# Performance work log

Hardware: AMD Instinct MI355X
Metric: run time of the kernel (lower is better)

The kernel has to match this reference:

```python
import jax, jax.numpy as jnp
import numpy as np

B, T, C = 2, 2048, 2048
H = 16
D = C // H  # head_dim = 128
ROPE_BASE = 10000.0


def rope_cos_sin(seq_len, dim, dtype):
    inv_freq = 1.0 / (ROPE_BASE ** (jnp.arange(0, dim, 2, dtype=jnp.float32) / dim))
    t = jnp.arange(seq_len, dtype=jnp.float32)
    freqs = jnp.outer(t, inv_freq)              # [T, D/2]
    emb = jnp.concatenate([freqs, freqs], -1)   # [T, D]
    return emb.astype(dtype), None  # placeholder replaced below


def rotate_half(x):
    x1, x2 = jnp.split(x, 2, axis=-1)
    return jnp.concatenate([-x2, x1], axis=-1)


def setup_inputs() -> dict:
    key = jax.random.key(0)
    k1, k2, k3 = jax.random.split(key, 3)
    sc = 1.0 / np.sqrt(C)
    x = jax.random.normal(k1, (B, T, C), dtype=jnp.float32)
    w_qkv = jax.random.normal(k2, (C, 3 * C), dtype=jnp.float32) * sc
    w_out = jax.random.normal(k3, (C, C), dtype=jnp.float32) * sc
    return {"x": x, "w_qkv": w_qkv, "w_out": w_out}


def reference(x, w_qkv, w_out):
    Bq, Tq, Cq = x.shape
    qkv = x @ w_qkv                                    # [B,T,3C]
    q, k, v = jnp.split(qkv, 3, axis=-1)
    # [B,T,C] -> [B,H,T,D]
    q = q.reshape(Bq, Tq, H, D).transpose(0, 2, 1, 3)
    k = k.reshape(Bq, Tq, H, D).transpose(0, 2, 1, 3)
    v = v.reshape(Bq, Tq, H, D).transpose(0, 2, 1, 3)
    # RoPE
    inv_freq = 1.0 / (ROPE_BASE ** (jnp.arange(0, D, 2, dtype=jnp.float32) / D))
    freqs = jnp.outer(jnp.arange(Tq, dtype=jnp.float32), inv_freq)  # [T, D/2]
    emb = jnp.concatenate([freqs, freqs], -1)                        # [T, D]
    cos = jnp.cos(emb).astype(x.dtype)[None, None]                   # [1,1,T,D]
    sin = jnp.sin(emb).astype(x.dtype)[None, None]
    q = q * cos + rotate_half(q) * sin
    k = k * cos + rotate_half(k) * sin
    # causal SDPA
    scale = 1.0 / np.sqrt(D)
    att = jnp.einsum("bhqd,bhkd->bhqk", q, k) * scale
    causal = jnp.tril(jnp.ones((Tq, Tq), dtype=bool))
    att = jnp.where(causal[None, None], att, -jnp.inf)
    att = jax.nn.softmax(att, axis=-1)
    y = jnp.einsum("bhqk,bhkd->bhqd", att, v)          # [B,H,T,D]
    y = y.transpose(0, 2, 1, 3).reshape(Bq, Tq, Cq)
    return y @ w_out
```

## Files before the change

### kernel.cpp

```cpp
#include <hip/hip_runtime.h>
#include <hip/hip_bf16.h>
#include <type_traits>
#include <utility>

typedef unsigned short u16;
typedef unsigned int u32;

#define B_ 2
#define T_ 2048
#define C_ 2048
#define H_ 16
#define D_ 128
#define LDQKV 6144

typedef float float4v __attribute__((ext_vector_type(4)));
typedef short short8 __attribute__((ext_vector_type(8)));

__device__ inline u16 f2bf(float f) {
  u32 u = __builtin_bit_cast(u32, f);
  u32 r = u + 0x7fffu + ((u >> 16) & 1u);
  return (u16)(r >> 16);
}
__device__ inline float bfbits2f(u16 b) {
  return __builtin_bit_cast(float, (u32)b << 16);
}
__device__ inline u32 pack2bf(float a, float b) {
  u32 ua = (__builtin_bit_cast(u32, a) + 0x8000u) >> 16;
  u32 ub = (__builtin_bit_cast(u32, b) + 0x8000u) & 0xffff0000u;
  return ua | ub;
}

#if defined(__HIP_DEVICE_COMPILE__)
typedef __bf16 bf16x8 __attribute__((ext_vector_type(8)));

template <typename V, typename = void>
struct mfma_takes_short : std::false_type {};
template <typename V>
struct mfma_takes_short<V, std::void_t<decltype(__builtin_amdgcn_mfma_f32_16x16x32_bf16(
    std::declval<V>(), std::declval<V>(), std::declval<float4v>(), 0, 0, 0))>>
    : std::true_type {};

template <typename SV>
__device__ inline float4v mfma_bf16(SV a, SV b, float4v c) {
  if constexpr (mfma_takes_short<SV>::value) {
    return __builtin_amdgcn_mfma_f32_16x16x32_bf16(a, b, c, 0, 0, 0);
  } else {
    return __builtin_amdgcn_mfma_f32_16x16x32_bf16(
        __builtin_bit_cast(bf16x8, a), __builtin_bit_cast(bf16x8, b), c, 0, 0, 0);
  }
}

__device__ inline void async16(u16* lds, const u16* g) {
  typedef __attribute__((address_space(3))) void lds_void;
  typedef __attribute__((address_space(1))) const void g_void;
  __builtin_amdgcn_global_load_lds((g_void*)g, (lds_void*)lds, 16, 0, 0);
}
#endif

__global__ __launch_bounds__(256) void cast_f32_bf16(const float* __restrict__ s,
                                                     u16* __restrict__ d) {
  int i = (blockIdx.x * 256 + threadIdx.x) * 4;
  float4 v = *(const float4*)(s + i);
  alignas(8) u16 o[4] = {f2bf(v.x), f2bf(v.y), f2bf(v.z), f2bf(v.w)};
  *(uint2*)(d + i) = *(const uint2*)o;
}

__global__ __launch_bounds__(256) void castT_f32_bf16(const float* __restrict__ src,
                                                      u16* __restrict__ dst,
                                                      int R, int Cc) {
  __shared__ float tile[32][33];
  const int t = threadIdx.x;
  const int r0 = blockIdx.y * 32, c0 = blockIdx.x * 32;
  const int lr = t >> 3, lc = (t & 7) * 4;
  float4 v = *(const float4*)(src + (size_t)(r0 + lr) * Cc + c0 + lc);
  tile[lr][lc + 0] = v.x;
  tile[lr][lc + 1] = v.y;
  tile[lr][lc + 2] = v.z;
  tile[lr][lc + 3] = v.w;
  __syncthreads();
  alignas(8) u16 o[4];
#pragma unroll
  for (int j = 0; j < 4; ++j) o[j] = f2bf(tile[lc + j][lr]);
  *(uint2*)(dst + (size_t)(c0 + lr) * R + r0 + lc) = *(const uint2*)o;
}

__global__ __launch_bounds__(256) void vT_build(const u16* __restrict__ qkv,
                                                u16* __restrict__ Vt) {
  __shared__ u16 lt[64][72];
  const int tid = threadIdx.x;
  const int bh = blockIdx.x;
  const int tt = blockIdx.y;
  const int dd = blockIdx.z;
  const int b = bh >> 4, h = bh & 15;
  const int r = tid >> 2;
  const int c4 = (tid & 3) * 16;
  const u16* src = qkv + ((size_t)(b * T_ + tt * 64 + r)) * LDQKV + 2 * C_ + h * 128 + dd * 64 + c4;
  *(uint4*)&lt[r][c4] = *(const uint4*)src;
  *(uint4*)&lt[r][c4 + 8] = *(const uint4*)(src + 8);
  __syncthreads();
  alignas(16) u16 o[16];
#pragma unroll
  for (int j = 0; j < 16; ++j) o[j] = lt[c4 + j][r];
  u16* dst = Vt + ((size_t)(bh * 128 + dd * 64 + r)) * 2048 + tt * 64 + c4;
  *(uint4*)dst = *(const uint4*)o;
  *(uint4*)(dst + 8) = *(const uint4*)(o + 8);
}

template <bool CF32>
__global__ __launch_bounds__(256) void gemm_bt(const u16* __restrict__ A,
                                               const u16* __restrict__ BT,
                                               void* __restrict__ Cp,
                                               int K, int lda, int ldbt, int ldc) {
#if defined(__HIP_DEVICE_COMPILE__)
  __shared__ u16 As[4096];
  __shared__ u16 Bs[4096];
  const int tid = threadIdx.x;
  const int lane = tid & 63;
  const int w = tid >> 6;
  const int wm = w & 1, wn = w >> 1;
  const int ml = lane & 15, qd = lane >> 4;
  const int m0 = blockIdx.y * 128, n0 = blockIdx.x * 128;
  const int sm = lane >> 2, sk = (lane & 3) * 8;
  const u16* gA[2];
  const u16* gB[2];
  u16 *lA[2], *lB[2];
#pragma unroll
  for (int r = 0; r < 2; ++r) {
    int seg = r * 4 + w;
    gA[r] = A + (size_t)(m0 + seg * 16 + sm) * lda + sk;
    gB[r] = BT + (size_t)(n0 + seg * 16 + sm) * ldbt + sk;
    lA[r] = As + seg * 512;
    lB[r] = Bs + seg * 512;
  }
  float4v acc[4][4] = {};
  for (int kk = 0; kk < K; kk += 32) {
    __syncthreads();
    async16(lA[0], gA[0] + kk);
    async16(lA[1], gA[1] + kk);
    async16(lB[0], gB[0] + kk);
    async16(lB[1], gB[1] + kk);
    __syncthreads();
    short8 a[4], b[4];
#pragma unroll
    for (int mt = 0; mt < 4; ++mt)
      a[mt] = *(const short8*)(As + (wm * 64 + mt * 16 + ml) * 32 + qd * 8);
#pragma unroll
    for (int nt = 0; nt < 4; ++nt)
      b[nt] = *(const short8*)(Bs + (wn * 64 + nt * 16 + ml) * 32 + qd * 8);
#pragma unroll
    for (int mt = 0; mt < 4; ++mt)
#pragma unroll
      for (int nt = 0; nt < 4; ++nt) acc[mt][nt] = mfma_bf16(a[mt], b[nt], acc[mt][nt]);
  }
#pragma unroll
  for (int mt = 0; mt < 4; ++mt) {
#pragma unroll
    for (int nt = 0; nt < 4; ++nt) {
#pragma unroll
      for (int r = 0; r < 4; ++r) {
        int row = m0 + wm * 64 + mt * 16 + qd * 4 + r;
        int col = n0 + wn * 64 + nt * 16 + ml;
        if constexpr (CF32) {
          ((float*)Cp)[(size_t)row * ldc + col] = acc[mt][nt][r];
        } else {
          ((u16*)Cp)[(size_t)row * ldc + col] = f2bf(acc[mt][nt][r]);
        }
      }
    }
  }
#endif
}

template <bool AF32, bool BF32, bool CF32>
__global__ __launch_bounds__(256) void gemm_mixed(const void* __restrict__ Ap,
                                                  const void* __restrict__ Bp,
                                                  void* __restrict__ Cp,
                                                  int M, int N, int K,
                                                  int lda, int ldb, int ldc) {
#if defined(__HIP_DEVICE_COMPILE__)
  __shared__ u16 As[64][40];
  __shared__ u16 Bs[64][40];
  const int tid = threadIdx.x;
  const int lane = tid & 63;
  const int w = tid >> 6;
  const int m0 = blockIdx.y * 64;
  const int n0 = blockIdx.x * 64;
  const int arow = tid >> 2, acol = (tid & 3) * 8;
  const int brow = tid >> 3, bcol = (tid & 7) * 8;
  const int ml = lane & 15, qd = lane >> 4;
  float4v acc[4] = {};
  for (int kk = 0; kk < K; kk += 32) {
    __syncthreads();
    if constexpr (AF32) {
      const float* A = (const float*)Ap;
      const float* src = A + (size_t)(m0 + arow) * lda + (kk + acol);
      float4 f0 = *(const float4*)src;
      float4 f1 = *(const float4*)(src + 4);
      alignas(16) u16 tmp[8] = {f2bf(f0.x), f2bf(f0.y), f2bf(f0.z), f2bf(f0.w),
                                f2bf(f1.x), f2bf(f1.y), f2bf(f1.z), f2bf(f1.w)};
      *(uint4*)(&As[arow][acol]) = *(const uint4*)tmp;
    } else {
      const u16* A = (const u16*)Ap;
      *(uint4*)(&As[arow][acol]) = *(const uint4*)(A + (size_t)(m0 + arow) * lda + (kk + acol));
    }
    if constexpr (BF32) {
      const float* Bm = (const float*)Bp;
      const float* src = Bm + (size_t)(kk + brow) * ldb + (n0 + bcol);
      float4 f0 = *(const float4*)src;
      float4 f1 = *(const float4*)(src + 4);
      float fv[8] = {f0.x, f0.y, f0.z, f0.w, f1.x, f1.y, f1.z, f1.w};
#pragma unroll
      for (int i = 0; i < 8; ++i) Bs[bcol + i][brow] = f2bf(fv[i]);
    } else {
      const u16* Bm = (const u16*)Bp;
      uint4 bv = *(const uint4*)(Bm + (size_t)(kk + brow) * ldb + (n0 + bcol));
      const u16* bsp = (const u16*)&bv;
#pragma unroll
      for (int i = 0; i < 8; ++i) Bs[bcol + i][brow] = bsp[i];
    }
    __syncthreads();
    short8 af = *(const short8*)(&As[w * 16 + ml][qd * 8]);
#pragma unroll
    for (int nt = 0; nt < 4; ++nt) {
      short8 bf = *(const short8*)(&Bs[nt * 16 + ml][qd * 8]);
      acc[nt] = mfma_bf16(af, bf, acc[nt]);
    }
  }
#pragma unroll
  for (int nt = 0; nt < 4; ++nt) {
#pragma unroll
    for (int r = 0; r < 4; ++r) {
      int row = m0 + w * 16 + qd * 4 + r;
      int col = n0 + nt * 16 + ml;
      if constexpr (CF32) {
        ((float*)Cp)[(size_t)row * ldc + col] = acc[nt][r];
      } else {
        ((u16*)Cp)[(size_t)row * ldc + col] = f2bf(acc[nt][r]);
      }
    }
  }
#endif
}

__global__ __launch_bounds__(256) void rope_inplace(u16* __restrict__ qkv, float qscale) {
  int idx = blockIdx.x * 256 + threadIdx.x;
  int d = idx & 63;
  int h = (idx >> 6) & 15;
  int t = (idx >> 10) & 2047;
  int b = idx >> 21;
  size_t row = (size_t)(b * T_ + t) * LDQKV;
  u16* qp = qkv + row + h * 128;
  u16* kp = qkv + row + C_ + h * 128;
  float q1 = bfbits2f(qp[d]);
  float q2 = bfbits2f(qp[d + 64]);
  float k1 = bfbits2f(kp[d]);
  float k2 = bfbits2f(kp[d + 64]);
  float invf = exp2f((float)d * -0.20762050593046012f);
  float fr = (float)t * invf;
  float sn, cs;
  sincosf(fr, &sn, &cs);
  qp[d] = f2bf((q1 * cs - q2 * sn) * qscale);
  qp[d + 64] = f2bf((q2 * cs + q1 * sn) * qscale);
  kp[d] = f2bf(k1 * cs - k2 * sn);
  kp[d + 64] = f2bf(k2 * cs + k1 * sn);
}

__global__ __launch_bounds__(256, 2) void attn_fwd2(u16* __restrict__ qkv,
                                                    const u16* __restrict__ Vt) {
#if defined(__HIP_DEVICE_COMPILE__)
  __shared__ alignas(16) u16 kS[64 * 128];
  __shared__ alignas(16) u16 vS[128 * 64];
  __shared__ alignas(16) u16 pS[4][32][72];
  const int tid = threadIdx.x;
  const int lane = tid & 63;
  const int w = tid >> 6;
  const int ml = lane & 15, qd = lane >> 4;
  const int gx = blockIdx.x;
  const int half = gx >> 8, rem = gx & 255;
  const int bh = rem >> 3, q3 = rem & 7;
  const int qt = half ? q3 : (15 - q3);
  const int b = bh >> 4, h = bh & 15;
  const int hc = h * 128;
  const int m0 = qt * 128;
  const size_t rb = (size_t)(b * T_);
  short8 qf[2][4];
#pragma unroll
  for (int m = 0; m < 2; ++m) {
    const u16* qp = qkv + (rb + m0 + w * 32 + m * 16 + ml) * LDQKV + hc;
#pragma unroll
    for (int k4 = 0; k4 < 4; ++k4) qf[m][k4] = *(const short8*)(qp + k4 * 32 + qd * 8);
  }
  float4v acc[2][8] = {};
  float mi[2] = {-1.0e30f, -1.0e30f}, li[2] = {0.f, 0.f};
  const int nchunk = 2 * qt + 2;
  const int krow0 = w * 16 + qd;
  const int vd0 = w * 32 + (lane >> 3);
  const int vsegoff = ((lane & 7) ^ (lane >> 3)) * 8;
  const size_t vtbase = ((size_t)bh * 128) * 2048;

  for (int c = 0; c < nchunk; ++c) {
    __syncthreads();
#pragma unroll
    for (int i = 0; i < 4; ++i) {
      int key = krow0 + i * 4;
      int seg = (ml ^ (i * 4 + qd)) * 8;
      async16(kS + (w * 4 + i) * 512,
              qkv + (rb + c * 64 + key) * LDQKV + C_ + hc + seg);
    }
#pragma unroll
    for (int i = 0; i < 4; ++i) {
      int d = vd0 + i * 8;
      async16(vS + (w * 4 + i) * 512,
              Vt + vtbase + (size_t)d * 2048 + c * 64 + vsegoff);
    }
    __syncthreads();
    if (c * 64 > m0 + w * 32 + 31) continue;
    float4v s[4][2] = {};
#pragma unroll
    for (int kt = 0; kt < 4; ++kt) {
#pragma unroll
      for (int k4 = 0; k4 < 4; ++k4) {
        int key = kt * 16 + ml;
        int slot = key * 16 + ((k4 * 4 + qd) ^ key);
        short8 kf = *(const short8*)(kS + ((kt * 16 + ml) * 16 + ((k4 * 4 + qd) ^ ml)) * 8);
        (void)key; (void)slot;
        s[kt][0] = mfma_bf16(kf, qf[0][k4], s[kt][0]);
        s[kt][1] = mfma_bf16(kf, qf[1][k4], s[kt][1]);
      }
    }
    const bool domask = (c * 64 + 63) > (m0 + w * 32);
    float alpha[2];
#pragma unroll
    for (int m = 0; m < 2; ++m) {
      int qrow = m0 + w * 32 + m * 16 + ml;
      if (domask) {
#pragma unroll
        for (int kt = 0; kt < 4; ++kt)
#pragma unroll
          for (int r = 0; r < 4; ++r) {
            int key = c * 64 + kt * 16 + qd * 4 + r;
            if (key > qrow) s[kt][m][r] = -1.0e30f;
          }
      }
      float mx = -1.0e30f;
#pragma unroll
      for (int kt = 0; kt < 4; ++kt)
#pragma unroll
        for (int r = 0; r < 4; ++r) mx = fmaxf(mx, s[kt][m][r]);
      mx = fmaxf(mx, __shfl_xor(mx, 16, 64));
      mx = fmaxf(mx, __shfl_xor(mx, 32, 64));
      float mnew = fmaxf(mi[m], mx);
      float a = __expf(mi[m] - mnew);
      float sm = 0.f;
#pragma unroll
      for (int kt = 0; kt < 4; ++kt)
#pragma unroll
        for (int r = 0; r < 4; ++r) {
          float p = __expf(s[kt][m][r] - mnew);
          s[kt][m][r] = p;
          sm += p;
        }
      sm += __shfl_xor(sm, 16, 64);
      sm += __shfl_xor(sm, 32, 64);
      li[m] = li[m] * a + sm;
      mi[m] = mnew;
      alpha[m] = a;
#pragma unroll
      for (int kt = 0; kt < 4; ++kt) {
        uint2 pk;
        pk.x = pack2bf(s[kt][m][0], s[kt][m][1]);
        pk.y = pack2bf(s[kt][m][2], s[kt][m][3]);
        *(uint2*)&pS[w][m * 16 + ml][kt * 16 + qd * 4] = pk;
      }
    }
#pragma unroll
    for (int m = 0; m < 2; ++m) {
#pragma unroll
      for (int r = 0; r < 4; ++r) {
        float aq = __shfl(alpha[m], qd * 4 + r, 64);
#pragma unroll
        for (int dt = 0; dt < 8; ++dt) acc[m][dt][r] *= aq;
      }
    }
#pragma unroll
    for (int k2 = 0; k2 < 2; ++k2) {
      short8 pa0 = *(const short8*)&pS[w][ml][k2 * 32 + qd * 8];
      short8 pa1 = *(const short8*)&pS[w][16 + ml][k2 * 32 + qd * 8];
#pragma unroll
      for (int dt = 0; dt < 8; ++dt) {
        int d = dt * 16 + ml;
        short8 vf = *(const short8*)(vS + (d * 8 + ((k2 * 4 + qd) ^ (ml & 7))) * 8);
        acc[0][dt] = mfma_bf16(pa0, vf, acc[0][dt]);
        acc[1][dt] = mfma_bf16(pa1, vf, acc[1][dt]);
      }
    }
  }
#pragma unroll
  for (int m = 0; m < 2; ++m) {
#pragma unroll
    for (int r = 0; r < 4; ++r) {
      float inv = 1.0f / __shfl(li[m], qd * 4 + r, 64);
      size_t row = rb + m0 + w * 32 + m * 16 + qd * 4 + r;
#pragma unroll
      for (int dt = 0; dt < 8; ++dt)
        qkv[row * LDQKV + hc + dt * 16 + ml] = f2bf(acc[m][dt][r] * inv);
    }
  }
#endif
}

__global__ __launch_bounds__(256, 2) void attn_fwd(u16* __restrict__ qkv) {
#if defined(__HIP_DEVICE_COMPILE__)
  __shared__ alignas(16) u16 ks[64][136];
  __shared__ alignas(16) u16 vt[128][72];
  __shared__ alignas(16) u16 pb[4][32][72];
  const int tid = threadIdx.x;
  const int lane = tid & 63;
  const int w = tid >> 6;
  const int ml = lane & 15, qd = lane >> 4;
  const int gx = blockIdx.x;
  const int half = gx >> 8;
  const int rem = gx & 255;
  const int bh = rem >> 3;
  const int q3 = rem & 7;
  const int qt = half ? q3 : (15 - q3);
  const int b = bh >> 4, h = bh & 15;
  const int hc = h * 128;
  const int m0 = qt * 128;
  const size_t rb = (size_t)(b * T_);
  short8 qf[2][4];
#pragma unroll
  for (int m = 0; m < 2; ++m) {
    const u16* qp = qkv + (rb + m0 + w * 32 + m * 16 + ml) * LDQKV + hc;
#pragma unroll
    for (int k4 = 0; k4 < 4; ++k4) qf[m][k4] = *(const short8*)(qp + k4 * 32 + qd * 8);
  }
  float4v acc[2][8] = {};
  float mi[2][4], li[2][4];
#pragma unroll
  for (int m = 0; m < 2; ++m)
#pragma unroll
    for (int r = 0; r < 4; ++r) { mi[m][r] = -1.0e30f; li[m][r] = 0.f; }
  const float scale = 0.08838834764831845f;
  const int srow = tid >> 2;
  const int scol = (tid & 3) * 32;
  const int nchunk = 2 * qt + 2;
  for (int c = 0; c < nchunk; ++c) {
    __syncthreads();
    {
      const u16* kp = qkv + (rb + c * 64 + srow) * LDQKV + C_ + hc + scol;
      const u16* vp = qkv + (rb + c * 64 + srow) * LDQKV + 2 * C_ + hc + scol;
#pragma unroll
      for (int i = 0; i < 4; ++i)
        *(uint4*)&ks[srow][scol + i * 8] = *(const uint4*)(kp + i * 8);
#pragma unroll
      for (int i = 0; i < 4; ++i) {
        uint4 vv = *(const uint4*)(vp + i * 8);
        const u16* e = (const u16*)&vv;
#pragma unroll
        for (int t = 0; t < 8; ++t) vt[scol + i * 8 + t][srow] = e[t];
      }
    }
    __syncthreads();
    if (c * 64 > m0 + w * 32 + 31) continue;
    float4v s[2][4] = {};
#pragma unroll
    for (int t = 0; t < 4; ++t) {
#pragma unroll
      for (int k4 = 0; k4 < 4; ++k4) {
        short8 bf = *(const short8*)(&ks[t * 16 + ml][k4 * 32 + qd * 8]);
        s[0][t] = mfma_bf16(qf[0][k4], bf, s[0][t]);
        s[1][t] = mfma_bf16(qf[1][k4], bf, s[1][t]);
      }
    }
    const bool domask = (c * 64 + 63) > (m0 + w * 32);
#pragma unroll
    for (int m = 0; m < 2; ++m) {
      float al[4];
#pragma unroll
      for (int r = 0; r < 4; ++r) {
        float x0 = s[m][0][r] * scale;
        float x1 = s[m][1][r] * scale;
        float x2 = s[m][2][r] * scale;
        float x3 = s[m][3][r] * scale;
        if (domask) {
          int row = m0 + w * 32 + m * 16 + qd * 4 + r;
          int j0 = c * 64 + ml;
          if (j0 > row) x0 = -1.0e30f;
          if (j0 + 16 > row) x1 = -1.0e30f;
          if (j0 + 32 > row) x2 = -1.0e30f;
          if (j0 + 48 > row) x3 = -1.0e30f;
        }
        float mx = fmaxf(fmaxf(x0, x1), fmaxf(x2, x3));
        mx = fmaxf(mx, __shfl_xor(mx, 1));
        mx = fmaxf(mx, __shfl_xor(mx, 2));
        mx = fmaxf(mx, __shfl_xor(mx, 4));
        mx = fmaxf(mx, __shfl_xor(mx, 8));
        float mnew = fmaxf(mi[m][r], mx);
        float a = __expf(mi[m][r] - mnew);
        float p0 = __expf(x0 - mnew);
        float p1 = __expf(x1 - mnew);
        float p2 = __expf(x2 - mnew);
        float p3 = __expf(x3 - mnew);
        float sm = p0 + p1 + p2 + p3;
        sm += __shfl_xor(sm, 1);
        sm += __shfl_xor(sm, 2);
        sm += __shfl_xor(sm, 4);
        sm += __shfl_xor(sm, 8);
        li[m][r] = li[m][r] * a + sm;
        mi[m][r] = mnew;
        al[r] = a;
        int prow = m * 16 + qd * 4 + r;
        pb[w][prow][ml] = f2bf(p0);
        pb[w][prow][16 + ml] = f2bf(p1);
        pb[w][prow][32 + ml] = f2bf(p2);
        pb[w][prow][48 + ml] = f2bf(p3);
      }
#pragma unroll
      for (int d = 0; d < 8; ++d) {
        acc[m][d][0] *= al[0];
        acc[m][d][1] *= al[1];
        acc[m][d][2] *= al[2];
        acc[m][d][3] *= al[3];
      }
    }
#pragma unroll
    for (int k2 = 0; k2 < 2; ++k2) {
      short8 pa0 = *(const short8*)(&pb[w][ml][k2 * 32 + qd * 8]);
      short8 pa1 = *(const short8*)(&pb[w][16 + ml][k2 * 32 + qd * 8]);
#pragma unroll
      for (int d = 0; d < 8; ++d) {
        short8 vf = *(const short8*)(&vt[d * 16 + ml][k2 * 32 + qd * 8]);
        acc[0][d] = mfma_bf16(pa0, vf, acc[0][d]);
        acc[1][d] = mfma_bf16(pa1, vf, acc[1][d]);
      }
    }
  }
#pragma unroll
  for (int m = 0; m < 2; ++m) {
#pragma unroll
    for (int r = 0; r < 4; ++r) {
      float inv = 1.0f / li[m][r];
      size_t row = rb + m0 + w * 32 + m * 16 + qd * 4 + r;
#pragma unroll
      for (int d = 0; d < 8; ++d)
        qkv[row * LDQKV + hc + d * 16 + ml] = f2bf(acc[m][d][r] * inv);
    }
  }
#endif
}

extern "C" void kernel_launch(void* const* d_in, const int* in_sizes, int n_in,
                              void* d_out, int out_size, void* d_ws, size_t ws_size,
                              hipStream_t stream) {
  const float* x = (const float*)d_in[0];
  const float* wqkv = (const float*)d_in[1];
  const float* wout = (const float*)d_in[2];
  float* out = (float*)d_out;
  char* ws = (char*)d_ws;
  u16* qkv = (u16*)ws;

  const size_t MB = 1024 * 1024;
  if (ws_size >= 96 * MB) {
    u16* xb = (u16*)(ws + 48 * MB);
    u16* wqkvT = (u16*)(ws + 64 * MB);
    u16* Vt = (u16*)(ws + 64 * MB);
    u16* woutT = (u16*)(ws + 88 * MB);
    cast_f32_bf16<<<dim3(8192), dim3(256), 0, stream>>>(x, xb);
    castT_f32_bf16<<<dim3(192, 64), dim3(256), 0, stream>>>(wqkv, wqkvT, 2048, 6144);
    castT_f32_bf16<<<dim3(64, 64), dim3(256), 0, stream>>>(wout, woutT, 2048, 2048);
    gemm_bt<false><<<dim3(48, 32), dim3(256), 0, stream>>>(
        xb, wqkvT, qkv, 2048, 2048, 2048, 6144);
    rope_inplace<<<dim3(16384), dim3(256), 0, stream>>>(qkv, 0.08838834764831845f);
    vT_build<<<dim3(32, 32, 2), dim3(256), 0, stream>>>(qkv, Vt);
    attn_fwd2<<<dim3(512), dim3(256), 0, stream>>>(qkv, Vt);
    gemm_bt<true><<<dim3(16, 32), dim3(256), 0, stream>>>(
        qkv, woutT, out, 2048, 6144, 2048, 2048);
  } else {
    gemm_mixed<true, true, false><<<dim3(96, 64), dim3(256), 0, stream>>>(
        x, wqkv, qkv, 4096, 6144, 2048, 2048, 6144, 6144);
    rope_inplace<<<dim3(16384), dim3(256), 0, stream>>>(qkv, 1.0f);
    attn_fwd<<<dim3(512), dim3(256), 0, stream>>>(qkv);
    gemm_mixed<false, true, true><<<dim3(32, 64), dim3(256), 0, stream>>>(
        qkv, wout, out, 4096, 2048, 2048, 6144, 2048, 2048);
  }
}
```

Before: 429.3 us.

## Add 256x256 ping-pong async-LDS GEMM for QKV projection

Replaces the 128x128-tile QKV projection GEMM with a new 256x256-tile kernel using 512 threads. It stages tiles through double-buffered shared memory via async global-to-LDS copies with XOR swizzling, and interleaves staging with MFMA under barriers and s_setprio. It also remaps workgroups with an XCD-aware swizzle. The aim is more data reuse per tile, with global-load latency hidden behind compute. The costs are 128 KB of LDS per block, which limits occupancy, and a grid of only 384 workgroups.

```diff
diff --git a/kernel.cpp b/kernel.cpp
--- a/kernel.cpp
+++ b/kernel.cpp
@@ -104,6 +104,164 @@
   u16* dst = Vt + ((size_t)(bh * 128 + dd * 64 + r)) * 2048 + tt * 64 + c4;
   *(uint4*)dst = *(const uint4*)o;
   *(uint4*)(dst + 8) = *(const uint4*)(o + 8);
+}
+
+template <bool CF32>
+__global__ __launch_bounds__(512, 2) void gemm256_bt(const u16* __restrict__ A,
+                                                     const u16* __restrict__ BT,
+                                                     void* __restrict__ Cp,
+                                                     int K, int lda, int ldbt, int ldc,
+                                                     int nbx) {
+#if defined(__HIP_DEVICE_COMPILE__)
+  __shared__ alignas(16) u16 As[2][256 * 64];
+  __shared__ alignas(16) u16 Bs[2][256 * 64];
+  const int tid = threadIdx.x;
+  const int lane = tid & 63;
+  const int w = tid >> 6;
+  const int wm = w >> 2, wn = w & 3;
+  const int ml = lane & 15, qd = lane >> 4;
+  const int nwg = gridDim.x;
+  const int cpx = nwg >> 3;
+  const int swz = (blockIdx.x & 7) * cpx + (blockIdx.x >> 3);
+  const int by = swz / nbx, bx = swz - by * nbx;
+  const int m0 = by * 256, n0 = bx * 256;
+  const int rowoff = lane >> 3;
+  const int chunk = ((lane & 7) ^ rowoff) * 8;
+  int rA0[2], rA1[2], rB0[2], rB1[2];
+#pragma unroll
+  for (int j = 0; j < 2; ++j) {
+    int g = w * 2 + j;
+    rA0[j] = (g >> 3) * 128 + (g & 7) * 8;
+    rA1[j] = (g >> 3) * 128 + 64 + (g & 7) * 8;
+    rB0[j] = (g >> 2) * 64 + (g & 3) * 8;
+    rB1[j] = (g >> 2) * 64 + 32 + (g & 3) * 8;
+  }
+  const int ntiles = K >> 6;
+  const int niter = ntiles >> 1;
+
+#define STG_A(bufi, h, kt)                                                       \
+  do {                                                                           \
+    async16(&As[bufi][rA##h[0] * 64],                                            \
+            A + (size_t)(m0 + rA##h[0] + rowoff) * lda + (kt) * 64 + chunk);     \
+    async16(&As[bufi][rA##h[1] * 64],                                            \
+            A + (size_t)(m0 + rA##h[1] + rowoff) * lda + (kt) * 64 + chunk);     \
+  } while (0)
+#define STG_B(bufi, h, kt)                                                       \
+  do {                                                                           \
+    async16(&Bs[bufi][rB##h[0] * 64],                                            \
+            BT + (size_t)(n0 + rB##h[0] + rowoff) * ldbt + (kt) * 64 + chunk);   \
+    async16(&Bs[bufi][rB##h[1] * 64],                                            \
+            BT + (size_t)(n0 + rB##h[1] + rowoff) * ldbt + (kt) * 64 + chunk);   \
+  } while (0)
+#define LDA8(bufi, mh)                                                           \
+  do {                                                                           \
+    _Pragma("unroll") for (int mt_ = 0; mt_ < 4; ++mt_)                          \
+    _Pragma("unroll") for (int ks_ = 0; ks_ < 2; ++ks_)                          \
+      a[mt_][ks_] = *(const short8*)&As[bufi][                                   \
+          (wm * 128 + (mh) * 64 + mt_ * 16 + ml) * 64 +                          \
+          (((qd + ks_ * 4) ^ (ml & 7)) * 8)];                                    \
+  } while (0)
+#define LDB4(bufi, nh)                                                           \
+  do {                                                                           \
+    _Pragma("unroll") for (int nt_ = 0; nt_ < 2; ++nt_)                          \
+    _Pragma("unroll") for (int ks_ = 0; ks_ < 2; ++ks_)                          \
+      b[nt_][ks_] = *(const short8*)&Bs[bufi][                                   \
+          (wn * 64 + (nh) * 32 + nt_ * 16 + ml) * 64 +                           \
+          (((qd + ks_ * 4) ^ (ml & 7)) * 8)];                                    \
+  } while (0)
+#define MMA16(mh, nh)                                                            \
+  do {                                                                           \
+    __builtin_amdgcn_s_setprio(1);                                               \
+    _Pragma("unroll") for (int ks_ = 0; ks_ < 2; ++ks_)                          \
+    _Pragma("unroll") for (int mt_ = 0; mt_ < 4; ++mt_)                          \
+    _Pragma("unroll") for (int nt_ = 0; nt_ < 2; ++nt_)                          \
+      acc[(mh) * 4 + mt_][(nh) * 2 + nt_] = mfma_bf16(                           \
+          a[mt_][ks_], b[nt_][ks_], acc[(mh) * 4 + mt_][(nh) * 2 + nt_]);        \
+    __builtin_amdgcn_s_setprio(0);                                               \
+  } while (0)
+#define BAR __builtin_amdgcn_s_barrier()
+#define LGKM0 asm volatile("s_waitcnt lgkmcnt(0)" ::: "memory")
+#define LGKM8 asm volatile("s_waitcnt lgkmcnt(8)" ::: "memory")
+#define VM4 asm volatile("s_waitcnt vmcnt(4)" ::: "memory")
+
+  float4v acc[8][4] = {};
+  short8 a[4][2], b[2][2];
+
+  STG_A(0, 0, 0);
+  STG_B(0, 0, 0);
+  STG_A(0, 1, 0);
+  STG_B(0, 1, 0);
+  STG_A(1, 0, 1);
+  STG_B(1, 0, 1);
+  VM4;
+  BAR;
+
+  for (int i = 0; i < niter; ++i) {
+    const int tb = 2 * i + 1;
+    const int t2 = (2 * i + 2 < ntiles) ? 2 * i + 2 : ntiles - 1;
+    const int t3 = (2 * i + 3 < ntiles) ? 2 * i + 3 : ntiles - 1;
+    LDA8(0, 0);
+    LDB4(0, 0);
+    STG_A(1, 1, tb);
+    LGKM8;
+    BAR; LGKM0; MMA16(0, 0); BAR;
+    LDB4(0, 1);
+    STG_B(1, 1, tb);
+    BAR; LGKM0; MMA16(0, 1); BAR;
+    LDA8(0, 1);
+    LDB4(0, 0);
+    STG_A(0, 0, t2);
+    LGKM8;
+    BAR; LGKM0; MMA16(1, 0); BAR;
+    LDB4(0, 1);
+    STG_B(0, 0, t2);
+    VM4;
+    BAR; LGKM0; MMA16(1, 1); BAR;
+    LDA8(1, 0);
+    LDB4(1, 0);
+    STG_A(0, 1, t2);
+    LGKM8;
+    BAR; LGKM0; MMA16(0, 0); BAR;
+    LDB4(1, 1);
+    STG_B(0, 1, t2);
+    BAR; LGKM0; MMA16(0, 1); BAR;
+    LDA8(1, 1);
+    LDB4(1, 0);
+    STG_A(1, 0, t3);
+    LGKM8;
+    BAR; LGKM0; MMA16(1, 0); BAR;
+    LDB4(1, 1);
+    STG_B(1, 0, t3);
+    VM4;
+    BAR; LGKM0; MMA16(1, 1); BAR;
+  }
+
+#pragma unroll
+  for (int mt = 0; mt < 8; ++mt) {
+#pragma unroll
+    for (int nt = 0; nt < 4; ++nt) {
+#pragma unroll
+      for (int r = 0; r < 4; ++r) {
+        int row = m0 + wm * 128 + mt * 16 + qd * 4 + r;
+        int col = n0 + wn * 64 + nt * 16 + ml;
+        if constexpr (CF32) {
+          ((float*)Cp)[(size_t)row * ldc + col] = acc[mt][nt][r];
+        } else {
+          ((u16*)Cp)[(size_t)row * ldc + col] = f2bf(acc[mt][nt][r]);
+        }
+      }
+    }
+  }
+#undef STG_A
+#undef STG_B
+#undef LDA8
+#undef LDB4
+#undef MMA16
+#undef BAR
+#undef LGKM0
+#undef LGKM8
+#undef VM4
+#endif
 }
 
 template <bool CF32>
@@ -569,8 +727,8 @@
     cast_f32_bf16<<<dim3(8192), dim3(256), 0, stream>>>(x, xb);
     castT_f32_bf16<<<dim3(192, 64), dim3(256), 0, stream>>>(wqkv, wqkvT, 2048, 6144);
     castT_f32_bf16<<<dim3(64, 64), dim3(256), 0, stream>>>(wout, woutT, 2048, 2048);
-    gemm_bt<false><<<dim3(48, 32), dim3(256), 0, stream>>>(
-        xb, wqkvT, qkv, 2048, 2048, 2048, 6144);
+    gemm256_bt<false><<<dim3(384), dim3(512), 0, stream>>>(
+        xb, wqkvT, qkv, 2048, 2048, 2048, 6144, 24);
     rope_inplace<<<dim3(16384), dim3(256), 0, stream>>>(qkv, 0.08838834764831845f);
     vT_build<<<dim3(32, 32, 2), dim3(256), 0, stream>>>(qkv, Vt);
     attn_fwd2<<<dim3(512), dim3(256), 0, stream>>>(qkv, Vt);
```

Measured after the change: 428.3 us. Within noise of the previous version (-0.2%).
